# Kernel optimization log

Measured on AMD Instinct MI355X. Metric: run time of the kernel, lower is better.

The kernel has to match this reference:

```python
import jax, jax.numpy as jnp
import numpy as np

N = 50000
E = 800000
IN_DIM = 128
HID = 64
H1 = 4
H2 = 2
OUT = 8
NEG_SLOPE = 0.2


def _p(key, shape, scale):
    return jax.random.normal(key, shape, dtype=jnp.float32) * scale


def setup_inputs() -> dict:
    key = jax.random.key(0)
    ks = jax.random.split(key, 20)
    d = {
        "x": jax.random.normal(ks[0], (N, IN_DIM), dtype=jnp.float32),
        "edge_index": jax.random.randint(ks[1], (2, E), 0, N, dtype=jnp.int64),
        # conv_feat: GATConv(IN_DIM, HID, heads=H1, concat=True)
        "W_feat": _p(ks[2], (IN_DIM, H1 * HID), 1.0 / np.sqrt(IN_DIM)),
        "a_src_feat": _p(ks[3], (H1, HID), 0.1),
        "a_dst_feat": _p(ks[4], (H1, HID), 0.1),
        "b_feat": jnp.zeros((H1 * HID,), dtype=jnp.float32),
        # node_att_mlp: Linear(HID*H1, 2)
        "W_mlp": _p(ks[5], (H1 * HID, 2), 1.0 / np.sqrt(H1 * HID)),
        "b_mlp": jnp.zeros((2,), dtype=jnp.float32),
        # objects_convs: GATConv(HID*H1, OUT, heads=H2, concat=False)
        "W_obj": _p(ks[6], (H1 * HID, H2 * OUT), 1.0 / np.sqrt(H1 * HID)),
        "a_src_obj": _p(ks[7], (H2, OUT), 0.1),
        "a_dst_obj": _p(ks[8], (H2, OUT), 0.1),
        "b_obj": jnp.zeros((OUT,), dtype=jnp.float32),
        # context_convs
        "W_ctx": _p(ks[9], (H1 * HID, H2 * OUT), 1.0 / np.sqrt(H1 * HID)),
        "a_src_ctx": _p(ks[10], (H2, OUT), 0.1),
        "a_dst_ctx": _p(ks[11], (H2, OUT), 0.1),
        "b_ctx": jnp.zeros((OUT,), dtype=jnp.float32),
        # context_objects_convs
        "W_co": _p(ks[12], (H1 * HID, H2 * OUT), 1.0 / np.sqrt(H1 * HID)),
        "a_src_co": _p(ks[13], (H2, OUT), 0.1),
        "a_dst_co": _p(ks[14], (H2, OUT), 0.1),
        "b_co": jnp.zeros((OUT,), dtype=jnp.float32),
    }
    return d


def gat_conv(x, src, dst, W, a_src, a_dst, b, heads, out_ch, concat):
    """PyG GATConv (eval mode, self-loops already included in src/dst)."""
    n = x.shape[0]
    h = (x @ W).reshape(n, heads, out_ch)               # [N,H,C]
    al_s = jnp.einsum('nhc,hc->nh', h, a_src)           # [N,H]
    al_d = jnp.einsum('nhc,hc->nh', h, a_dst)
    e = jax.nn.leaky_relu(al_s[src] + al_d[dst], NEG_SLOPE)  # [E,H]
    # destination-grouped softmax
    m = jax.ops.segment_max(e, dst, num_segments=n)
    p = jnp.exp(e - m[dst])
    s = jax.ops.segment_sum(p, dst, num_segments=n)
    alpha = p / (s[dst] + 1e-16)                        # [E,H]
    msg = h[src] * alpha[:, :, None]                    # [E,H,C]
    out = jax.ops.segment_sum(msg, dst, num_segments=n) # [N,H,C]
    if concat:
        return out.reshape(n, heads * out_ch) + b
    return out.mean(axis=1) + b


def reference(x, edge_index, W_feat, a_src_feat, a_dst_feat, b_feat,
              W_mlp, b_mlp, W_obj, a_src_obj, a_dst_obj, b_obj,
              W_ctx, a_src_ctx, a_dst_ctx, b_ctx,
              W_co, a_src_co, a_dst_co, b_co):
    n = x.shape[0]
    loops = jnp.arange(n, dtype=edge_index.dtype)
    src = jnp.concatenate([edge_index[0], loops])
    dst = jnp.concatenate([edge_index[1], loops])

    # conv_feat + ELU (eval mode: dropout is identity; args.layers == 0 so no convs loop)
    h = jax.nn.elu(gat_conv(x, src, dst, W_feat, a_src_feat, a_dst_feat, b_feat, H1, HID, True))

    node_att = jax.nn.softmax(h @ W_mlp + b_mlp, axis=-1)   # [N,2]
    xo = node_att[:, 0:1] * h
    xc = node_att[:, 1:2] * h

    xo_logis = jax.nn.log_softmax(
        gat_conv(xo, src, dst, W_obj, a_src_obj, a_dst_obj, b_obj, H2, OUT, False), axis=-1)
    xc_logis = jax.nn.log_softmax(
        gat_conv(xc, src, dst, W_ctx, a_src_ctx, a_dst_ctx, b_ctx, H2, OUT, False), axis=-1)
    # with_random=False -> random_idx is identity; cat_or_add='add'
    xco = xc + xo
    xco_logis = jax.nn.log_softmax(
        gat_conv(xco, src, dst, W_co, a_src_co, a_dst_co, b_co, H2, OUT, False), axis=-1)

    return (xo_logis, xc_logis, xco_logis, jax.nn.elu(xo), jax.nn.elu(xc))
```

## Files before the change

### kernel.cpp

```cpp
#include <hip/hip_runtime.h>
#include <hip/hip_bf16.h>
#include <hip/hip_fp16.h>

#define N_NODES 50000
#define N_EDGES 800000
#define ET (N_EDGES + N_NODES)
#define IN_DIM 128
#define F1 256
#define H1 4
#define HID 64
#define H2 2
#define OUTC 8
#define F2 16

typedef unsigned short u16;
typedef unsigned int u32;

static __device__ __forceinline__ float lrelu(float x) { return x > 0.f ? x : 0.2f * x; }
static __device__ __forceinline__ float eluf(float x) { return x > 0.f ? x : __expf(x) - 1.f; }
static __device__ __forceinline__ u16 f2h(float x) {
    __half h = __float2half(x);
    return *reinterpret_cast<u16*>(&h);
}

__global__ void zero_kernel(int* p, int n) {
    int i = blockIdx.x * blockDim.x + threadIdx.x;
    if (i < n) p[i] = 0;
}

__global__ void hist_kernel(const int* __restrict__ ei, int* __restrict__ deg) {
    int e = blockIdx.x * blockDim.x + threadIdx.x;
    if (e >= ET) return;
    int dst = (e < N_EDGES) ? ei[N_EDGES + e] : (e - N_EDGES);
    atomicAdd(&deg[dst], 1);
}

#define SCAN_NT 1024
__global__ __launch_bounds__(SCAN_NT) void scan_kernel(int* __restrict__ deg,
                                                       int* __restrict__ off) {
    __shared__ int sums[SCAN_NT];
    const int ITEMS = (N_NODES + SCAN_NT - 1) / SCAN_NT;
    int t = threadIdx.x;
    int base = t * ITEMS;
    int s = 0;
    for (int i = 0; i < ITEMS; i++) {
        int idx = base + i;
        if (idx < N_NODES) s += deg[idx];
    }
    sums[t] = s;
    __syncthreads();
    for (int d = 1; d < SCAN_NT; d <<= 1) {
        int v = (t >= d) ? sums[t - d] : 0;
        __syncthreads();
        sums[t] += v;
        __syncthreads();
    }
    int run = (t == 0) ? 0 : sums[t - 1];
    for (int i = 0; i < ITEMS; i++) {
        int idx = base + i;
        if (idx < N_NODES) {
            int v = deg[idx];
            off[idx] = run;
            deg[idx] = run;
            run += v;
        }
    }
    if (t == SCAN_NT - 1) off[N_NODES] = run;
}

__global__ void scatter_kernel(const int* __restrict__ ei, int* __restrict__ cursor,
                               int* __restrict__ csr_src) {
    int e = blockIdx.x * blockDim.x + threadIdx.x;
    if (e >= ET) return;
    int src, dst;
    if (e < N_EDGES) {
        src = ei[e];
        dst = ei[N_EDGES + e];
    } else {
        src = dst = e - N_EDGES;
    }
    int pos = atomicAdd(&cursor[dst], 1);
    csr_src[pos] = src;
}

__global__ void wt_kernel(const float* __restrict__ W_obj, const float* __restrict__ W_ctx,
                          const float* __restrict__ W_co, const float* __restrict__ W_mlp,
                          float* __restrict__ WTi) {
    int t = blockIdx.x * blockDim.x + threadIdx.x;
    if (t >= 64 * 256) return;
    int c = t >> 8;
    int k = t & 255;
    float v = 0.f;
    if (c < 16) v = W_obj[k * 16 + c];
    else if (c < 32) v = W_ctx[k * 16 + (c - 16)];
    else if (c < 48) v = W_co[k * 16 + (c - 32)];
    else if (c < 50) v = W_mlp[k * 2 + (c - 48)];
    WTi[(k >> 2) * 256 + c * 4 + (k & 3)] = v;
}

__global__ __launch_bounds__(256) void gemm1_kernel(const float* __restrict__ x,
                                                    const float* __restrict__ Wf,
                                                    const float* __restrict__ a_src,
                                                    const float* __restrict__ a_dst,
                                                    u16* __restrict__ h_fp,
                                                    float* __restrict__ al_s,
                                                    float* __restrict__ al_d) {
    __shared__ float xt[32 * 128];
    int tid = threadIdx.x;
    int node0 = blockIdx.x * 32;
    const float4* xg = reinterpret_cast<const float4*>(x) + (size_t)node0 * 32;
    float4* xt4 = reinterpret_cast<float4*>(xt);
    int maxf4 = (N_NODES - node0) * 32;
#pragma unroll
    for (int i = 0; i < 4; i++) {
        int f4 = tid + i * 256;
        float4 v = make_float4(0.f, 0.f, 0.f, 0.f);
        if (f4 < maxf4) v = xg[f4];
        xt4[f4] = v;
    }
    __syncthreads();

    float acc[32];
#pragma unroll
    for (int r = 0; r < 32; r++) acc[r] = 0.f;
    int j = tid;
    for (int kc = 0; kc < 128; kc += 8) {
        float w[8];
#pragma unroll
        for (int kk = 0; kk < 8; kk++) w[kk] = Wf[(kc + kk) * 256 + j];
#pragma unroll
        for (int r = 0; r < 32; r++) {
            float4 a0 = xt4[r * 32 + (kc >> 2)];
            float4 a1 = xt4[r * 32 + (kc >> 2) + 1];
            acc[r] += a0.x * w[0] + a0.y * w[1] + a0.z * w[2] + a0.w * w[3] +
                      a1.x * w[4] + a1.y * w[5] + a1.z * w[6] + a1.w * w[7];
        }
    }

    {
        int head = tid >> 6;
        int lane = tid & 63;
        float asv = a_src[head * 64 + lane];
        float adv = a_dst[head * 64 + lane];
        for (int r = 0; r < 32; r++) {
            float ps = acc[r] * asv;
            float pd = acc[r] * adv;
#pragma unroll
            for (int d = 1; d < 64; d <<= 1) {
                ps += __shfl_xor(ps, d);
                pd += __shfl_xor(pd, d);
            }
            int node = node0 + r;
            if (lane == 0 && node < N_NODES) {
                al_s[node * 4 + head] = ps;
                al_d[node * 4 + head] = pd;
            }
        }
    }

    __syncthreads();
    u16* hs = reinterpret_cast<u16*>(xt);
    int headj = tid >> 6, chj = tid & 63;
#pragma unroll
    for (int r = 0; r < 32; r++) hs[r * 256 + chj * 4 + headj] = f2h(acc[r]);
    __syncthreads();
    uint2* hq = reinterpret_cast<uint2*>(h_fp);
    const uint2* hsq = reinterpret_cast<const uint2*>(hs);
#pragma unroll
    for (int it = 0; it < 8; it++) {
        int idx = it * 256 + tid;
        int node_local = idx >> 6;
        if (node0 + node_local < N_NODES) hq[(size_t)node0 * 64 + idx] = hsq[idx];
    }
}

__global__ __launch_bounds__(256) void conv1_aggregate(const int* __restrict__ deg_off,
                                                       const int* __restrict__ csr_src,
                                                       const u16* __restrict__ h_fp,
                                                       const float* __restrict__ al_s,
                                                       const float* __restrict__ al_d,
                                                       const float* __restrict__ b_feat,
                                                       float* __restrict__ h1) {
    int wave = threadIdx.x >> 6;
    int lane = threadIdx.x & 63;
    int node = blockIdx.x * 4 + wave;
    if (node >= N_NODES) return;
    int beg = deg_off[node], end = deg_off[node + 1];
    float4 aldv = *reinterpret_cast<const float4*>(al_d + node * 4);
    const uint2* hq = reinterpret_cast<const uint2*>(h_fp);
    float acc0 = 0.f, acc1 = 0.f, acc2 = 0.f, acc3 = 0.f;
    float s0 = 0.f, s1 = 0.f, s2 = 0.f, s3 = 0.f;

    int k = beg;
    for (; k + 4 <= end; k += 4) {
        int sa = csr_src[k], sb = csr_src[k + 1], sc = csr_src[k + 2], sd = csr_src[k + 3];
        float4 Aa = *reinterpret_cast<const float4*>(al_s + sa * 4);
        float4 Ab = *reinterpret_cast<const float4*>(al_s + sb * 4);
        float4 Ac = *reinterpret_cast<const float4*>(al_s + sc * 4);
        float4 Ad = *reinterpret_cast<const float4*>(al_s + sd * 4);
        uint2 ha = hq[(size_t)sa * 64 + lane];
        uint2 hb = hq[(size_t)sb * 64 + lane];
        uint2 hc = hq[(size_t)sc * 64 + lane];
        uint2 hd = hq[(size_t)sd * 64 + lane];
#define C1_EDGE(A, h)                                                        \
        {                                                                    \
            float p0 = __expf(lrelu(A.x + aldv.x));                          \
            float p1 = __expf(lrelu(A.y + aldv.y));                          \
            float p2 = __expf(lrelu(A.z + aldv.z));                          \
            float p3 = __expf(lrelu(A.w + aldv.w));                          \
            s0 += p0; s1 += p1; s2 += p2; s3 += p3;                          \
            __half2 q01 = *reinterpret_cast<const __half2*>(&h.x);           \
            __half2 q23 = *reinterpret_cast<const __half2*>(&h.y);           \
            acc0 += p0 * __low2float(q01);                                   \
            acc1 += p1 * __high2float(q01);                                  \
            acc2 += p2 * __low2float(q23);                                   \
            acc3 += p3 * __high2float(q23);                                  \
        }
        C1_EDGE(Aa, ha)
        C1_EDGE(Ab, hb)
        C1_EDGE(Ac, hc)
        C1_EDGE(Ad, hd)
    }
    for (; k < end; k++) {
        int sa = csr_src[k];
        float4 Aa = *reinterpret_cast<const float4*>(al_s + sa * 4);
        uint2 ha = hq[(size_t)sa * 64 + lane];
        C1_EDGE(Aa, ha)
    }
#undef C1_EDGE
    h1[(size_t)node * 256 + 0 * 64 + lane] = eluf(acc0 / (s0 + 1e-16f) + b_feat[0 * 64 + lane]);
    h1[(size_t)node * 256 + 1 * 64 + lane] = eluf(acc1 / (s1 + 1e-16f) + b_feat[1 * 64 + lane]);
    h1[(size_t)node * 256 + 2 * 64 + lane] = eluf(acc2 / (s2 + 1e-16f) + b_feat[2 * 64 + lane]);
    h1[(size_t)node * 256 + 3 * 64 + lane] = eluf(acc3 / (s3 + 1e-16f) + b_feat[3 * 64 + lane]);
}

__global__ __launch_bounds__(256) void phaseB_kernel(
    const float* __restrict__ h1, const float* __restrict__ WTi, const float* __restrict__ b_mlp,
    const float* __restrict__ as_obj, const float* __restrict__ ad_obj,
    const float* __restrict__ as_ctx, const float* __restrict__ ad_ctx,
    const float* __restrict__ as_co, const float* __restrict__ ad_co,
    u32* __restrict__ pack2, float* __restrict__ ald2,
    float* __restrict__ out_xo, float* __restrict__ out_xc) {
    __shared__ float hts[32 * 256];
    __shared__ float dots[32][52];
    int tid = threadIdx.x;
    int node0 = blockIdx.x * 32;
    int lane = tid & 63;
    int rg = tid >> 6;
    const float4* WTi4 = reinterpret_cast<const float4*>(WTi);
    const float4* hg = reinterpret_cast<const float4*>(h1) + (size_t)node0 * 64;
    float4* hts4 = reinterpret_cast<float4*>(hts);

    int maxf4 = (N_NODES - node0) * 64;
#pragma unroll
    for (int i = 0; i < 8; i++) {
        int idx = tid + i * 256;
        float4 v = make_float4(0.f, 0.f, 0.f, 0.f);
        if (idx < maxf4) v = hg[idx];
        hts4[idx] = v;
    }
    __syncthreads();

    float accd[8];
#pragma unroll
    for (int r = 0; r < 8; r++) accd[r] = 0.f;
#pragma unroll 2
    for (int k4 = 0; k4 < 64; k4++) {
        float4 wv = WTi4[k4 * 64 + lane];
#pragma unroll
        for (int r = 0; r < 8; r++) {
            float4 hv = hts4[(rg * 8 + r) * 64 + k4];
            accd[r] += hv.x * wv.x + hv.y * wv.y + hv.z * wv.z + hv.w * wv.w;
        }
    }
    if (lane < 50) {
#pragma unroll
        for (int r = 0; r < 8; r++) dots[rg * 8 + r][lane] = accd[r];
    }
    __syncthreads();

    if (tid < 32) {
        int r = tid;
        float l0 = dots[r][48] + b_mlp[0];
        float l1 = dots[r][49] + b_mlp[1];
        float mx = fmaxf(l0, l1);
        float e0 = __expf(l0 - mx), e1 = __expf(l1 - mx);
        float inv = 1.f / (e0 + e1);
        dots[r][50] = e0 * inv;
        dots[r][51] = e1 * inv;
    }
    __syncthreads();

    {
        int r = tid >> 3, j = tid & 7;
        int node = node0 + r;
        if (node < N_NODES) {
            float a0 = dots[r][50], a1 = dots[r][51];
            u32* pb = pack2 + (size_t)node * 32;
#pragma unroll
            for (int wi = 0; wi < 3; wi++) {
                int w = j + wi * 8;
                int c0 = 2 * w;
                int v = c0 >> 4;
                float scale = (v == 0) ? a0 : ((v == 1) ? a1 : 1.f);
                float g0 = dots[r][c0] * scale;
                float g1 = dots[r][c0 + 1] * scale;
                __half2 hh = __halves2half2(__float2half(g0), __float2half(g1));
                pb[w] = *reinterpret_cast<u32*>(&hh);
            }
            if (j < 6) {
                int v = j >> 1, head = j & 1;
                float scale = (v == 0) ? a0 : ((v == 1) ? a1 : 1.f);
                const float* asp = (v == 0) ? as_obj : ((v == 1) ? as_ctx : as_co);
                const float* adp = (v == 0) ? ad_obj : ((v == 1) ? ad_ctx : ad_co);
                float ss = 0.f, dd = 0.f;
#pragma unroll
                for (int i = 0; i < 8; i++) {
                    float g = dots[r][v * 16 + head * 8 + i] * scale;
                    ss += g * asp[head * 8 + i];
                    dd += g * adp[head * 8 + i];
                }
                pb[24 + j] = __float_as_uint(ss);
                ald2[(size_t)node * 8 + j] = dd;
            }
        }
    }
    __syncthreads();

    {
#pragma unroll
        for (int i = 0; i < 8; i++) {
            int idx = tid + i * 256;
            int r = idx >> 6, c4 = idx & 63;
            int node = node0 + r;
            if (node < N_NODES) {
                float4 hv = hts4[idx];
                float a0 = dots[r][50], a1 = dots[r][51];
                float4 xo4 = make_float4(eluf(a0 * hv.x), eluf(a0 * hv.y),
                                         eluf(a0 * hv.z), eluf(a0 * hv.w));
                float4 xc4 = make_float4(eluf(a1 * hv.x), eluf(a1 * hv.y),
                                         eluf(a1 * hv.z), eluf(a1 * hv.w));
                reinterpret_cast<float4*>(out_xo + (size_t)node * 256)[c4] = xo4;
                reinterpret_cast<float4*>(out_xc + (size_t)node * 256)[c4] = xc4;
            }
        }
    }
}

__global__ __launch_bounds__(256) void conv2_aggregate(const int* __restrict__ deg_off,
                                                       const int* __restrict__ csr_src,
                                                       const u32* __restrict__ pack2,
                                                       const float* __restrict__ ald2,
                                                       const float* __restrict__ b_obj,
                                                       const float* __restrict__ b_ctx,
                                                       const float* __restrict__ b_co,
                                                       float* __restrict__ out) {
    int wave = threadIdx.x >> 6;
    int lane = threadIdx.x & 63;
    int node = blockIdx.x * 4 + wave;
    if (node >= N_NODES) return;
    int v = lane >> 4;
    if (v > 2) v = 2;
    int head = (lane >> 3) & 1;
    int c = lane & 7;
    int aidx = v * 2 + head;
    int gword = (v * 16 + head * 8 + c) >> 1;
    int ghi = c & 1;
    const float* bb = (v == 0) ? b_obj : (v == 1) ? b_ctx : b_co;
    float ald = ald2[(size_t)node * 8 + aidx];
    int beg = deg_off[node], end = deg_off[node + 1];
    float acc = 0.f, s = 0.f;
    int k = beg;
#define C2_EDGE(sx)                                                              \
    {                                                                            \
        const u32* pb = pack2 + (size_t)(sx) * 32;                               \
        u32 gw = pb[gword];                                                      \
        float als = __uint_as_float(pb[24 + aidx]);                              \
        __half2 gh = *reinterpret_cast<const __half2*>(&gw);                     \
        float g = ghi ? __high2float(gh) : __low2float(gh);                      \
        float p = __expf(lrelu(als + ald));                                      \
        s += p;                                                                  \
        acc += p * g;                                                            \
    }
    for (; k + 4 <= end; k += 4) {
        int sa = csr_src[k], sb = csr_src[k + 1], sc = csr_src[k + 2], sd = csr_src[k + 3];
        C2_EDGE(sa)
        C2_EDGE(sb)
        C2_EDGE(sc)
        C2_EDGE(sd)
    }
    for (; k < end; k++) {
        int sa = csr_src[k];
        C2_EDGE(sa)
    }
#undef C2_EDGE
    float o = acc / (s + 1e-16f);
    float mean = 0.5f * (o + __shfl_xor(o, 8)) + bb[c];
    float mx = mean;
#pragma unroll
    for (int d = 1; d < 8; d <<= 1) mx = fmaxf(mx, __shfl_xor(mx, d));
    float ex = __expf(mean - mx);
    float ss = ex;
#pragma unroll
    for (int d = 1; d < 8; d <<= 1) ss += __shfl_xor(ss, d);
    float res = (mean - mx) - __logf(ss);
    if (lane < 48 && head == 0) out[(size_t)v * (N_NODES * 8) + node * 8 + c] = res;
}

extern "C" void kernel_launch(void* const* d_in, const int* in_sizes, int n_in, void* d_out,
                              int out_size, void* d_ws, size_t ws_size, hipStream_t stream) {
    const float* x = (const float*)d_in[0];
    const int* ei = (const int*)d_in[1];
    const float* W_feat = (const float*)d_in[2];
    const float* a_src_feat = (const float*)d_in[3];
    const float* a_dst_feat = (const float*)d_in[4];
    const float* b_feat = (const float*)d_in[5];
    const float* W_mlp = (const float*)d_in[6];
    const float* b_mlp = (const float*)d_in[7];
    const float* W_obj = (const float*)d_in[8];
    const float* as_obj = (const float*)d_in[9];
    const float* ad_obj = (const float*)d_in[10];
    const float* b_obj = (const float*)d_in[11];
    const float* W_ctx = (const float*)d_in[12];
    const float* as_ctx = (const float*)d_in[13];
    const float* ad_ctx = (const float*)d_in[14];
    const float* b_ctx = (const float*)d_in[15];
    const float* W_co = (const float*)d_in[16];
    const float* as_co = (const float*)d_in[17];
    const float* ad_co = (const float*)d_in[18];
    const float* b_co = (const float*)d_in[19];
    float* out = (float*)d_out;

    char* w = (char*)d_ws;
    auto alloc = [&](size_t bytes) {
        void* p = (void*)w;
        w += (bytes + 255) & ~(size_t)255;
        return p;
    };
    int* cursor = (int*)alloc((size_t)N_NODES * 4);
    int* deg_off = (int*)alloc((size_t)(N_NODES + 1) * 4);
    int* csr_src = (int*)alloc((size_t)ET * 4);
    u16* h_fp = (u16*)alloc((size_t)N_NODES * 256 * 2);
    float* al_s1 = (float*)alloc((size_t)N_NODES * 4 * 4);
    float* al_d1 = (float*)alloc((size_t)N_NODES * 4 * 4);
    float* h1 = (float*)alloc((size_t)N_NODES * 256 * 4);
    float* WTi = (float*)alloc((size_t)64 * 256 * 4);
    u32* pack2 = (u32*)alloc((size_t)N_NODES * 32 * 4);
    float* ald2 = (float*)alloc((size_t)N_NODES * 8 * 4);

    float* out_xo_logis = out;
    float* out_xo = out + (size_t)3 * N_NODES * 8;
    float* out_xc = out_xo + (size_t)N_NODES * 256;

    zero_kernel<<<(N_NODES + 255) / 256, 256, 0, stream>>>(cursor, N_NODES);
    hist_kernel<<<(ET + 255) / 256, 256, 0, stream>>>(ei, cursor);
    scan_kernel<<<1, SCAN_NT, 0, stream>>>(cursor, deg_off);
    scatter_kernel<<<(ET + 255) / 256, 256, 0, stream>>>(ei, cursor, csr_src);
    wt_kernel<<<64, 256, 0, stream>>>(W_obj, W_ctx, W_co, W_mlp, WTi);

    gemm1_kernel<<<(N_NODES + 31) / 32, 256, 0, stream>>>(x, W_feat, a_src_feat, a_dst_feat,
                                                          h_fp, al_s1, al_d1);
    conv1_aggregate<<<(N_NODES + 3) / 4, 256, 0, stream>>>(deg_off, csr_src, h_fp, al_s1, al_d1,
                                                           b_feat, h1);
    phaseB_kernel<<<(N_NODES + 31) / 32, 256, 0, stream>>>(
        h1, WTi, b_mlp, as_obj, ad_obj, as_ctx, ad_ctx, as_co, ad_co, pack2, ald2, out_xo, out_xc);
    conv2_aggregate<<<(N_NODES + 3) / 4, 256, 0, stream>>>(deg_off, csr_src, pack2, ald2, b_obj,
                                                           b_ctx, b_co, out_xo_logis);
}
```

Measured before the change: 630.2 us.

## Replace single-block prefix scan with multi-block three-phase scan

The degree prefix sum used to run in one 1024-thread block, with each thread walking about 49 elements serially, so it used only a single CU. It now runs as three kernels: per-block wavefront-shuffle scans, a single-block scan of the 196 block sums, and an add pass that writes both the offsets and the scatter cursor. This spreads the work across the GPU and uses shuffles instead of a shared-memory log-step loop, at the cost of two extra kernel launches.

```diff
diff --git a/kernel.cpp b/kernel.cpp
--- a/kernel.cpp
+++ b/kernel.cpp
@@ -12,6 +12,7 @@
 #define H2 2
 #define OUTC 8
 #define F2 16
+#define NB_SCAN ((N_NODES + 255) / 256)
 
 typedef unsigned short u16;
 typedef unsigned int u32;
@@ -35,37 +36,61 @@
     atomicAdd(&deg[dst], 1);
 }
 
-#define SCAN_NT 1024
-__global__ __launch_bounds__(SCAN_NT) void scan_kernel(int* __restrict__ deg,
-                                                       int* __restrict__ off) {
-    __shared__ int sums[SCAN_NT];
-    const int ITEMS = (N_NODES + SCAN_NT - 1) / SCAN_NT;
+__global__ __launch_bounds__(256) void blockscan_kernel(const int* __restrict__ cnt,
+                                                        int* __restrict__ off,
+                                                        int* __restrict__ bsum) {
     int t = threadIdx.x;
-    int base = t * ITEMS;
-    int s = 0;
-    for (int i = 0; i < ITEMS; i++) {
-        int idx = base + i;
-        if (idx < N_NODES) s += deg[idx];
-    }
-    sums[t] = s;
-    __syncthreads();
-    for (int d = 1; d < SCAN_NT; d <<= 1) {
-        int v = (t >= d) ? sums[t - d] : 0;
-        __syncthreads();
-        sums[t] += v;
-        __syncthreads();
-    }
-    int run = (t == 0) ? 0 : sums[t - 1];
-    for (int i = 0; i < ITEMS; i++) {
-        int idx = base + i;
-        if (idx < N_NODES) {
-            int v = deg[idx];
-            off[idx] = run;
-            deg[idx] = run;
-            run += v;
-        }
-    }
-    if (t == SCAN_NT - 1) off[N_NODES] = run;
+    int b = blockIdx.x;
+    int idx = b * 256 + t;
+    int lane = t & 63, wv = t >> 6;
+    int val = (idx < N_NODES) ? cnt[idx] : 0;
+    int s = val;
+#pragma unroll
+    for (int d = 1; d < 64; d <<= 1) {
+        int v2 = __shfl_up(s, d);
+        if (lane >= d) s += v2;
+    }
+    __shared__ int wsum[4];
+    if (lane == 63) wsum[wv] = s;
+    __syncthreads();
+    int prefix = 0;
+#pragma unroll
+    for (int i = 0; i < 3; i++) prefix += (i < wv) ? wsum[i] : 0;
+    s += prefix;
+    if (idx < N_NODES) off[idx] = s - val;
+    if (t == 255) bsum[b] = s;
+}
+
+__global__ __launch_bounds__(256) void bsum_scan_kernel(int* __restrict__ bsum,
+                                                        int* __restrict__ off) {
+    int t = threadIdx.x;
+    int lane = t & 63, wv = t >> 6;
+    int val = (t < NB_SCAN) ? bsum[t] : 0;
+    int s = val;
+#pragma unroll
+    for (int d = 1; d < 64; d <<= 1) {
+        int v2 = __shfl_up(s, d);
+        if (lane >= d) s += v2;
+    }
+    __shared__ int wsum[4];
+    if (lane == 63) wsum[wv] = s;
+    __syncthreads();
+    int prefix = 0;
+#pragma unroll
+    for (int i = 0; i < 3; i++) prefix += (i < wv) ? wsum[i] : 0;
+    s += prefix;
+    if (t < NB_SCAN) bsum[t] = s - val;
+    if (t == 255) off[N_NODES] = s;
+}
+
+__global__ __launch_bounds__(256) void add_off_kernel(int* __restrict__ off,
+                                                      const int* __restrict__ bsum,
+                                                      int* __restrict__ cursor) {
+    int idx = blockIdx.x * 256 + threadIdx.x;
+    if (idx >= N_NODES) return;
+    int f = off[idx] + bsum[blockIdx.x];
+    off[idx] = f;
+    cursor[idx] = f;
 }
 
 __global__ void scatter_kernel(const int* __restrict__ ei, int* __restrict__ cursor,
@@ -440,6 +465,7 @@
     int* cursor = (int*)alloc((size_t)N_NODES * 4);
     int* deg_off = (int*)alloc((size_t)(N_NODES + 1) * 4);
     int* csr_src = (int*)alloc((size_t)ET * 4);
+    int* bsum = (int*)alloc((size_t)NB_SCAN * 4);
     u16* h_fp = (u16*)alloc((size_t)N_NODES * 256 * 2);
     float* al_s1 = (float*)alloc((size_t)N_NODES * 4 * 4);
     float* al_d1 = (float*)alloc((size_t)N_NODES * 4 * 4);
@@ -454,7 +480,9 @@
 
     zero_kernel<<<(N_NODES + 255) / 256, 256, 0, stream>>>(cursor, N_NODES);
     hist_kernel<<<(ET + 255) / 256, 256, 0, stream>>>(ei, cursor);
-    scan_kernel<<<1, SCAN_NT, 0, stream>>>(cursor, deg_off);
+    blockscan_kernel<<<NB_SCAN, 256, 0, stream>>>(cursor, deg_off, bsum);
+    bsum_scan_kernel<<<1, 256, 0, stream>>>(bsum, deg_off);
+    add_off_kernel<<<NB_SCAN, 256, 0, stream>>>(deg_off, bsum, cursor);
     scatter_kernel<<<(ET + 255) / 256, 256, 0, stream>>>(ei, cursor, csr_src);
     wt_kernel<<<64, 256, 0, stream>>>(W_obj, W_ctx, W_co, W_mlp, WTi);
 
```

After: 526.7 us. -16.4%, faster.
